# Kernel optimization log

Hardware: AMD Instinct MI355X
Metric: run time of the kernel (lower is better)

The kernel has to match this reference:

```python
import jax, jax.numpy as jnp
import numpy as np

B, N, C = 4, 4096, 1024
NUM_HEADS = 16
HEAD_DIM = C // NUM_HEADS


def setup_inputs() -> dict:
    key = jax.random.key(0)
    k1, k2, k3, k4 = jax.random.split(key, 4)
    s_in = 1.0 / np.sqrt(C)
    return {
        "x": jax.random.normal(k1, (B, N, C), dtype=jnp.float32),
        "H": 64,
        "W": 64,
        "Wqkv": jax.random.normal(k2, (3 * C, C), dtype=jnp.float32) * s_in,
        "Wproj": jax.random.normal(k3, (C, C), dtype=jnp.float32) * s_in,
        "bproj": jnp.zeros((C,), dtype=jnp.float32),
        "alpha": jnp.ones((NUM_HEADS,), dtype=jnp.float32),
    }


def reference(x, H, W, Wqkv, Wproj, bproj, alpha):
    Bb, Nn, Cc = x.shape
    h, d = NUM_HEADS, HEAD_DIM
    # qkv: [B, N, 3C] -> [3, B, h, N, d]
    qkv = jnp.einsum('bnc,oc->bno', x, Wqkv)
    qkv = qkv.reshape(Bb, Nn, 3, h, d).transpose(2, 0, 3, 1, 4)
    q, k, v = qkv[0], qkv[1], qkv[2]  # each [B, h, N, d]
    # channel attention: contract over tokens N -> [B, h, d, d]
    attn = jnp.einsum('bhnd,bhne->bhde', k, q) / alpha[None, :, None, None]
    attn = jax.nn.softmax(attn, axis=-1)
    # (dropout is identity in eval/reference mode)
    # head_out: [B, h, d, N] -> transpose -> [B, N, h, d] -> concat heads
    out = jnp.einsum('bhde,bhne->bhdn', attn, v)
    out = out.transpose(0, 3, 1, 2).reshape(Bb, Nn, Cc)
    return jnp.einsum('bnc,oc->bno', out, Wproj) + bproj
```

## Files before the change

kernel.cpp:

```cpp
#include <hip/hip_runtime.h>
#include <hip/hip_bf16.h>
#include <cstdint>
#include <cstddef>

typedef unsigned short u16;
typedef __bf16 bf16x8 __attribute__((ext_vector_type(8)));
typedef float f32x4 __attribute__((ext_vector_type(4)));
typedef unsigned short u16x4 __attribute__((ext_vector_type(4)));
typedef unsigned short u16x8 __attribute__((ext_vector_type(8)));

#define AS1(p) ((__attribute__((address_space(1))) void*)(p))
#define AS3(p) ((__attribute__((address_space(3))) void*)(p))

__device__ __forceinline__ float bf2f(u16 u) {
  unsigned v = ((unsigned)u) << 16; float f; __builtin_memcpy(&f, &v, 4); return f;
}
__device__ __forceinline__ u16 f2bf(float f) {
  unsigned u; __builtin_memcpy(&u, &f, 4);
  u += 0x7FFFu + ((u >> 16) & 1u);
  return (u16)(u >> 16);
}

__global__ __launch_bounds__(256) void convert_kernel(const float* __restrict__ src,
                                                      u16* __restrict__ dst, int n4) {
  int i = blockIdx.x * blockDim.x + threadIdx.x;
  int stride = gridDim.x * blockDim.x;
  for (; i < n4; i += stride) {
    float4 v = ((const float4*)src)[i];
    u16x4 o;
    o.x = f2bf(v.x); o.y = f2bf(v.y); o.z = f2bf(v.z); o.w = f2bf(v.w);
    ((u16x4*)dst)[i] = o;
  }
}

__global__ __launch_bounds__(256) void convert_split_kernel(const float* __restrict__ src,
                                                            u16* __restrict__ hi,
                                                            u16* __restrict__ lo, int n4) {
  int i = blockIdx.x * blockDim.x + threadIdx.x;
  int stride = gridDim.x * blockDim.x;
  for (; i < n4; i += stride) {
    float4 v = ((const float4*)src)[i];
    u16x4 oh, ol;
    oh.x = f2bf(v.x); ol.x = f2bf(v.x - bf2f(oh.x));
    oh.y = f2bf(v.y); ol.y = f2bf(v.y - bf2f(oh.y));
    oh.z = f2bf(v.z); ol.z = f2bf(v.z - bf2f(oh.z));
    oh.w = f2bf(v.w); ol.w = f2bf(v.w - bf2f(oh.w));
    ((u16x4*)hi)[i] = oh;
    ((u16x4*)lo)[i] = ol;
  }
}

__global__ __launch_bounds__(256) void transpose_split_kernel(const float* __restrict__ x,
                                                              u16* __restrict__ Xb,
                                                              u16* __restrict__ XThi,
                                                              u16* __restrict__ XTlo) {
  __shared__ u16 lhi[64 * 72];
  __shared__ u16 llo[64 * 72];
  const int t  = threadIdx.x;
  const int nT = blockIdx.x, cT = blockIdx.y, b = blockIdx.z;
  const size_t xbase = ((size_t)b * 4096 + nT * 64) * 1024 + cT * 64;
  const int c4 = (t & 15) * 4;
  const int r0 = t >> 4;
#pragma unroll
  for (int j = 0; j < 4; ++j) {
    int r = r0 + j * 16;
    float4 v = *(const float4*)(x + xbase + (size_t)r * 1024 + c4);
    u16x4 hi;
    hi.x = f2bf(v.x); hi.y = f2bf(v.y); hi.z = f2bf(v.z); hi.w = f2bf(v.w);
    *(u16x4*)(Xb + xbase + (size_t)r * 1024 + c4) = hi;
    u16 lo[4];
    lo[0] = f2bf(v.x - bf2f(hi.x)); lo[1] = f2bf(v.y - bf2f(hi.y));
    lo[2] = f2bf(v.z - bf2f(hi.z)); lo[3] = f2bf(v.w - bf2f(hi.w));
    u16 hia[4] = { hi.x, hi.y, hi.z, hi.w };
#pragma unroll
    for (int i = 0; i < 4; ++i) {
      lhi[(c4 + i) * 72 + r] = hia[i];
      llo[(c4 + i) * 72 + r] = lo[i];
    }
  }
  __syncthreads();
  const int c  = t >> 2;
  const int n0 = (t & 3) * 16;
  const size_t tbase = ((size_t)b * 1024 + cT * 64 + c) * 4096 + nT * 64 + n0;
  *(u16x8*)(XThi + tbase)     = *(const u16x8*)(lhi + c * 72 + n0);
  *(u16x8*)(XThi + tbase + 8) = *(const u16x8*)(lhi + c * 72 + n0 + 8);
  *(u16x8*)(XTlo + tbase)     = *(const u16x8*)(llo + c * 72 + n0);
  *(u16x8*)(XTlo + tbase + 8) = *(const u16x8*)(llo + c * 72 + n0 + 8);
}

template<bool OUT_BF16, bool HAS_BIAS>
__global__ __launch_bounds__(512, 2) void gemm_pipe(const u16* __restrict__ A,
                                                    const u16* __restrict__ B,
                                                    void* __restrict__ Cv,
                                                    const float* __restrict__ bias,
                                                    int M, int N, int K,
                                                    size_t sA, size_t sB, size_t sC) {
  __shared__ __align__(16) u16 lds[4][2][8192];
  const int tid  = threadIdx.x;
  const int lane = tid & 63;
  const int wave = tid >> 6;
  const int wm = wave >> 2, wn = wave & 3;
  const int rowTile = blockIdx.x * 256;
  const int colTile = blockIdx.y * 256;
  A += (size_t)blockIdx.z * sA;
  B += (size_t)blockIdx.z * sB;

  size_t srcA[2], srcB[2];
  int ldsOff[2];
#pragma unroll
  for (int j = 0; j < 2; ++j) {
    const int L = j * 512 + tid;
    const int sr = L >> 3;
    const int slot = (L & 7) ^ (sr & 7);
    const int r  = (sr << 1) | (slot >> 2);
    const int kq = slot & 3;
    srcA[j] = (size_t)(rowTile + r) * K + kq * 8;
    srcB[j] = (size_t)(colTile + r) * K + kq * 8;
    ldsOff[j] = (j * 512 + (tid & 448)) * 16;
  }

  const int m15 = lane & 15, kq4 = lane >> 4;
  const int r0a = wm * 128 + m15, sa0 = r0a >> 1;
  const int idxA0 = sa0 * 64 + (((((r0a & 1) << 2) | kq4)) ^ (sa0 & 7)) * 8;
  const int r0b = wn * 64 + m15, sb0 = r0b >> 1;
  const int idxB0 = sb0 * 64 + (((((r0b & 1) << 2) | kq4)) ^ (sb0 & 7)) * 8;

  const int NT = K >> 5;

  auto stageA = [&](int tt) {
    char* d = (char*)&lds[tt & 3][0][0];
    const int kt = tt << 5;
#pragma unroll
    for (int j = 0; j < 2; ++j)
      __builtin_amdgcn_global_load_lds(AS1(A + srcA[j] + kt), AS3(d + ldsOff[j]), 16, 0, 0);
  };
  auto stageB = [&](int tt) {
    char* d = (char*)&lds[tt & 3][1][0];
    const int kt = tt << 5;
#pragma unroll
    for (int j = 0; j < 2; ++j)
      __builtin_amdgcn_global_load_lds(AS1(B + srcB[j] + kt), AS3(d + ldsOff[j]), 16, 0, 0);
  };

  stageA(0); stageB(0);
  if (NT > 1) { stageA(1); stageB(1); }
  if (NT > 2) { stageA(2); stageB(2); }
  if (NT > 2) asm volatile("s_waitcnt vmcnt(8)" ::: "memory");
  else        asm volatile("s_waitcnt vmcnt(0)" ::: "memory");
  __builtin_amdgcn_sched_barrier(0);
  __builtin_amdgcn_s_barrier();
  __builtin_amdgcn_sched_barrier(0);

  f32x4 acc[8][4] = {};
  for (int t = 0; t < NT; ++t) {
    const u16* bufA = &lds[t & 3][0][0];
    const u16* bufB = &lds[t & 3][1][0];
    bf16x8 a[8], bfr[4];
#pragma unroll
    for (int ni = 0; ni < 4; ++ni) bfr[ni] = *(const bf16x8*)(bufB + idxB0 + ni * 512);
#pragma unroll
    for (int mi = 0; mi < 4; ++mi) a[mi] = *(const bf16x8*)(bufA + idxA0 + mi * 512);
    if (t + 3 < NT) stageA(t + 3);
    __builtin_amdgcn_sched_barrier(0);
    __builtin_amdgcn_s_barrier();
    __builtin_amdgcn_sched_barrier(0);
    __builtin_amdgcn_s_setprio(1);
#pragma unroll
    for (int mi = 0; mi < 4; ++mi)
#pragma unroll
      for (int ni = 0; ni < 4; ++ni)
        acc[mi][ni] = __builtin_amdgcn_mfma_f32_16x16x32_bf16(a[mi], bfr[ni], acc[mi][ni], 0, 0, 0);
    __builtin_amdgcn_s_setprio(0);
    __builtin_amdgcn_sched_barrier(0);
    __builtin_amdgcn_s_barrier();
    __builtin_amdgcn_sched_barrier(0);
#pragma unroll
    for (int mi = 4; mi < 8; ++mi) a[mi] = *(const bf16x8*)(bufA + idxA0 + mi * 512);
    if (t + 3 < NT) stageB(t + 3);
    __builtin_amdgcn_sched_barrier(0);
    __builtin_amdgcn_s_barrier();
    __builtin_amdgcn_sched_barrier(0);
    __builtin_amdgcn_s_setprio(1);
#pragma unroll
    for (int mi = 4; mi < 8; ++mi)
#pragma unroll
      for (int ni = 0; ni < 4; ++ni)
        acc[mi][ni] = __builtin_amdgcn_mfma_f32_16x16x32_bf16(a[mi], bfr[ni], acc[mi][ni], 0, 0, 0);
    __builtin_amdgcn_s_setprio(0);
    if (t < NT - 1) {
      if (t + 3 < NT)      asm volatile("s_waitcnt vmcnt(8)" ::: "memory");
      else if (t + 2 < NT) asm volatile("s_waitcnt vmcnt(4)" ::: "memory");
      else                 asm volatile("s_waitcnt vmcnt(0)" ::: "memory");
    }
    __builtin_amdgcn_sched_barrier(0);
    __builtin_amdgcn_s_barrier();
    __builtin_amdgcn_sched_barrier(0);
  }

  const int crow0 = rowTile + wm * 128 + (lane >> 4) * 4;
  const int ccol0 = colTile + wn * 64 + m15;
  if constexpr (OUT_BF16) {
    u16* C = (u16*)Cv + (size_t)blockIdx.z * sC;
#pragma unroll
    for (int mi = 0; mi < 8; ++mi)
#pragma unroll
      for (int ni = 0; ni < 4; ++ni) {
        const int col = ccol0 + ni * 16;
        const float bv = HAS_BIAS ? bias[col] : 0.f;
#pragma unroll
        for (int r = 0; r < 4; ++r)
          C[(size_t)(crow0 + mi * 16 + r) * N + col] = f2bf(acc[mi][ni][r] + bv);
      }
  } else {
    float* C = (float*)Cv + (size_t)blockIdx.z * sC;
#pragma unroll
    for (int mi = 0; mi < 8; ++mi)
#pragma unroll
      for (int ni = 0; ni < 4; ++ni) {
        const int col = ccol0 + ni * 16;
        const float bv = HAS_BIAS ? bias[col] : 0.f;
#pragma unroll
        for (int r = 0; r < 4; ++r)
          C[(size_t)(crow0 + mi * 16 + r) * N + col] = acc[mi][ni][r] + bv;
      }
  }
}

__global__ __launch_bounds__(256) void gemm_gram(const u16* __restrict__ XThi,
                                                 const u16* __restrict__ XTlo,
                                                 float* __restrict__ Gpart) {
  __shared__ __align__(16) u16 lAh[128 * 32];
  __shared__ __align__(16) u16 lAl[128 * 32];
  __shared__ __align__(16) u16 lBh[128 * 32];
  __shared__ __align__(16) u16 lBl[128 * 32];
  const int tid  = threadIdx.x;
  const int lane = tid & 63;
  const int wave = tid >> 6;
  const int wr = (wave >> 1) * 64;
  const int wc = (wave & 1) * 64;
  const int m  = lane & 15;
  const int ko = (lane >> 4) * 8;

  const int jx = blockIdx.x;
  const int b  = blockIdx.y;
  int rT, cT, slice, k0, kend;
  if (jx < 112) {
    const int tile = jx >> 2, kq = jx & 3;
    int t = tile, rt = 0;
    while (t >= 7 - rt) { t -= 7 - rt; ++rt; }
    const int ct = rt + 1 + t;
    rT = rt; cT = ct;
    if (kq >= 2) { rT = ct; cT = rt; }
    slice = kq & 1;
    k0 = kq * 1024; kend = k0 + 1024;
  } else {
    const int j2 = jx - 112;
    rT = cT = j2 >> 1;
    slice = j2 & 1;
    k0 = slice * 2048; kend = k0 + 2048;
  }
  const int rowTile = rT * 128, colTile = cT * 128;

  const u16* Ahp = XThi + ((size_t)b << 22);
  const u16* Alp = XTlo + ((size_t)b << 22);

  f32x4 acc[4][4] = {};
  for (int kt = k0; kt < kend; kt += 32) {
#pragma unroll
    for (int i = 0; i < 2; ++i) {
      int idx = i * 256 + tid;
      int row = idx >> 2;
      int kc  = (idx & 3) * 8;
      int ldsOff = (i * 256 + (tid & 192)) * 16;
      size_t aoff = (size_t)(rowTile + row) * 4096 + kt + kc;
      size_t boff = (size_t)(colTile + row) * 4096 + kt + kc;
      __builtin_amdgcn_global_load_lds(AS1(Ahp + aoff), AS3((char*)lAh + ldsOff), 16, 0, 0);
      __builtin_amdgcn_global_load_lds(AS1(Alp + aoff), AS3((char*)lAl + ldsOff), 16, 0, 0);
      __builtin_amdgcn_global_load_lds(AS1(Ahp + boff), AS3((char*)lBh + ldsOff), 16, 0, 0);
      __builtin_amdgcn_global_load_lds(AS1(Alp + boff), AS3((char*)lBl + ldsOff), 16, 0, 0);
    }
    __syncthreads();
    bf16x8 ah[4], al[4], bh[4], bl[4];
#pragma unroll
    for (int rb = 0; rb < 4; ++rb) {
      ah[rb] = *(const bf16x8*)(lAh + (wr + rb * 16 + m) * 32 + ko);
      al[rb] = *(const bf16x8*)(lAl + (wr + rb * 16 + m) * 32 + ko);
    }
#pragma unroll
    for (int cb = 0; cb < 4; ++cb) {
      bh[cb] = *(const bf16x8*)(lBh + (wc + cb * 16 + m) * 32 + ko);
      bl[cb] = *(const bf16x8*)(lBl + (wc + cb * 16 + m) * 32 + ko);
    }
#pragma unroll
    for (int rb = 0; rb < 4; ++rb)
#pragma unroll
      for (int cb = 0; cb < 4; ++cb) {
        acc[rb][cb] = __builtin_amdgcn_mfma_f32_16x16x32_bf16(ah[rb], bh[cb], acc[rb][cb], 0, 0, 0);
        acc[rb][cb] = __builtin_amdgcn_mfma_f32_16x16x32_bf16(ah[rb], bl[cb], acc[rb][cb], 0, 0, 0);
        acc[rb][cb] = __builtin_amdgcn_mfma_f32_16x16x32_bf16(al[rb], bh[cb], acc[rb][cb], 0, 0, 0);
      }
    __syncthreads();
  }

  float* out = Gpart + ((size_t)(slice * 4 + b) << 20);
  const int crow0 = rowTile + wr + (lane >> 4) * 4;
  const int ccol0 = colTile + wc + (lane & 15);
#pragma unroll
  for (int rb = 0; rb < 4; ++rb)
#pragma unroll
    for (int cb = 0; cb < 4; ++cb)
#pragma unroll
      for (int r = 0; r < 4; ++r)
        out[(size_t)(crow0 + rb * 16 + r) * 1024 + ccol0 + cb * 16] = acc[rb][cb][r];
}

__global__ __launch_bounds__(256) void gram_reduce_split(const float* __restrict__ Gp,
                                                         u16* __restrict__ Ghi,
                                                         u16* __restrict__ Glo) {
  const int rt = blockIdx.x, ct = blockIdx.y, b = blockIdx.z;
  const bool diag128 = (rt >> 1) == (ct >> 1);
  const float* s0 = Gp + ((size_t)b << 20);
  const float* s1 = Gp + ((size_t)(4 + b) << 20);
  __shared__ float lT[64 * 68];
  const int t = threadIdx.x;
  const int r = t >> 2;
  const int c16 = (t & 3) * 16;

  if (!diag128) {
    const size_t bb = (size_t)(ct * 64 + r) * 1024 + rt * 64 + c16;
#pragma unroll
    for (int q = 0; q < 4; ++q) {
      float4 v0 = *(const float4*)(s0 + bb + q * 4);
      float4 v1 = *(const float4*)(s1 + bb + q * 4);
      float4 s = { v0.x + v1.x, v0.y + v1.y, v0.z + v1.z, v0.w + v1.w };
      *(float4*)(lT + r * 68 + c16 + q * 4) = s;
    }
    __syncthreads();
  }

  const size_t ab = (size_t)(rt * 64 + r) * 1024 + ct * 64 + c16;
  const size_t ob = ((size_t)b << 20) + ab;
#pragma unroll
  for (int q = 0; q < 4; ++q) {
    float4 v0 = *(const float4*)(s0 + ab + q * 4);
    float4 v1 = *(const float4*)(s1 + ab + q * 4);
    float g[4] = { v0.x + v1.x, v0.y + v1.y, v0.z + v1.z, v0.w + v1.w };
    if (!diag128) {
#pragma unroll
      for (int i = 0; i < 4; ++i) g[i] += lT[(c16 + q * 4 + i) * 68 + r];
    }
    u16x4 oh, ol;
    oh.x = f2bf(g[0]); ol.x = f2bf(g[0] - bf2f(oh.x));
    oh.y = f2bf(g[1]); ol.y = f2bf(g[1] - bf2f(oh.y));
    oh.z = f2bf(g[2]); ol.z = f2bf(g[2] - bf2f(oh.z));
    oh.w = f2bf(g[3]); ol.w = f2bf(g[3] - bf2f(oh.w));
    *(u16x4*)(Ghi + ob + q * 4) = oh;
    *(u16x4*)(Glo + ob + q * 4) = ol;
  }
}

__global__ __launch_bounds__(256) void gemm_tprime(const u16* __restrict__ Wqh,
                                                   const u16* __restrict__ Wql,
                                                   const u16* __restrict__ Ghi,
                                                   const u16* __restrict__ Glo,
                                                   u16* __restrict__ Tph,
                                                   u16* __restrict__ Tpl) {
  __shared__ __align__(16) u16 lAh[128 * 32];
  __shared__ __align__(16) u16 lAl[128 * 32];
  __shared__ __align__(16) u16 lBh[128 * 32];
  __shared__ __align__(16) u16 lBl[128 * 32];
  const int tid  = threadIdx.x;
  const int lane = tid & 63;
  const int wave = tid >> 6;
  const int rowTile = blockIdx.x * 128;
  const int colTile = blockIdx.y * 128;
  const size_t zoff = (size_t)blockIdx.z << 20;
  const int wr = (wave >> 1) * 64;
  const int wc = (wave & 1) * 64;

  f32x4 acc[4][4] = {};
  const int m  = lane & 15;
  const int ko = (lane >> 4) * 8;

  for (int kt = 0; kt < 1024; kt += 32) {
#pragma unroll
    for (int i = 0; i < 2; ++i) {
      int idx = i * 256 + tid;
      int row = idx >> 2;
      int kc  = (idx & 3) * 8;
      int ldsOff = (i * 256 + (tid & 192)) * 16;
      size_t aoff = (size_t)(rowTile + row) * 1024 + kt + kc;
      size_t boff = zoff + (size_t)(colTile + row) * 1024 + kt + kc;
      __builtin_amdgcn_global_load_lds(AS1(Wqh + aoff), AS3((char*)lAh + ldsOff), 16, 0, 0);
      __builtin_amdgcn_global_load_lds(AS1(Wql + aoff), AS3((char*)lAl + ldsOff), 16, 0, 0);
      __builtin_amdgcn_global_load_lds(AS1(Ghi + boff), AS3((char*)lBh + ldsOff), 16, 0, 0);
      __builtin_amdgcn_global_load_lds(AS1(Glo + boff), AS3((char*)lBl + ldsOff), 16, 0, 0);
    }
    __syncthreads();
    bf16x8 ah[4], al[4], bh[4], bl[4];
#pragma unroll
    for (int rb = 0; rb < 4; ++rb) {
      ah[rb] = *(const bf16x8*)(lAh + (wr + rb * 16 + m) * 32 + ko);
      al[rb] = *(const bf16x8*)(lAl + (wr + rb * 16 + m) * 32 + ko);
    }
#pragma unroll
    for (int cb = 0; cb < 4; ++cb) {
      bh[cb] = *(const bf16x8*)(lBh + (wc + cb * 16 + m) * 32 + ko);
      bl[cb] = *(const bf16x8*)(lBl + (wc + cb * 16 + m) * 32 + ko);
    }
#pragma unroll
    for (int rb = 0; rb < 4; ++rb)
#pragma unroll
      for (int cb = 0; cb < 4; ++cb) {
        acc[rb][cb] = __builtin_amdgcn_mfma_f32_16x16x32_bf16(ah[rb], bh[cb], acc[rb][cb], 0, 0, 0);
        acc[rb][cb] = __builtin_amdgcn_mfma_f32_16x16x32_bf16(ah[rb], bl[cb], acc[rb][cb], 0, 0, 0);
        acc[rb][cb] = __builtin_amdgcn_mfma_f32_16x16x32_bf16(al[rb], bh[cb], acc[rb][cb], 0, 0, 0);
      }
    __syncthreads();
  }

  const int crow0 = rowTile + wr + (lane >> 4) * 4;
  const int ccol0 = colTile + wc + (lane & 15);
#pragma unroll
  for (int rb = 0; rb < 4; ++rb)
#pragma unroll
    for (int cb = 0; cb < 4; ++cb)
#pragma unroll
      for (int r = 0; r < 4; ++r) {
        float v = acc[rb][cb][r];
        u16 hi = f2bf(v);
        u16 lo = f2bf(v - bf2f(hi));
        size_t off = zoff + (size_t)(crow0 + rb * 16 + r) * 1024 + ccol0 + cb * 16;
        Tph[off] = hi;
        Tpl[off] = lo;
      }
}

__global__ __launch_bounds__(256) void s_softmax_kernel(const u16* __restrict__ Wqh,
                                                        const u16* __restrict__ Wql,
                                                        const u16* __restrict__ Tph,
                                                        const u16* __restrict__ Tpl,
                                                        const float* __restrict__ alpha,
                                                        u16* __restrict__ attnT) {
  const int h = blockIdx.x, b = blockIdx.y;
  const int tid = threadIdx.x, lane = tid & 63, wave = tid >> 6;
  __shared__ __align__(16) u16 lAh[64 * 32];
  __shared__ __align__(16) u16 lAl[64 * 32];
  __shared__ __align__(16) u16 lBh[64 * 32];
  __shared__ __align__(16) u16 lBl[64 * 32];

  const size_t aBase = (size_t)(1024 + h * 64) * 1024;
  const size_t bBase = ((size_t)b << 20) + (size_t)(h * 64) * 1024;

  f32x4 acc[4] = {};
  const int m  = lane & 15;
  const int ko = (lane >> 4) * 8;
  const int srow = tid >> 2;
  const int skc  = (tid & 3) * 8;
  const int ldsOff = (tid & 192) * 16;

  for (int kt = 0; kt < 1024; kt += 32) {
    __builtin_amdgcn_global_load_lds(AS1(Wqh + aBase + (size_t)srow * 1024 + kt + skc),
                                     AS3((char*)lAh + ldsOff), 16, 0, 0);
    __builtin_amdgcn_global_load_lds(AS1(Wql + aBase + (size_t)srow * 1024 + kt + skc),
                                     AS3((char*)lAl + ldsOff), 16, 0, 0);
    __builtin_amdgcn_global_load_lds(AS1(Tph + bBase + (size_t)srow * 1024 + kt + skc),
                                     AS3((char*)lBh + ldsOff), 16, 0, 0);
    __builtin_amdgcn_global_load_lds(AS1(Tpl + bBase + (size_t)srow * 1024 + kt + skc),
                                     AS3((char*)lBl + ldsOff), 16, 0, 0);
    __syncthreads();
    bf16x8 ah = *(const bf16x8*)(lAh + (wave * 16 + m) * 32 + ko);
    bf16x8 al = *(const bf16x8*)(lAl + (wave * 16 + m) * 32 + ko);
#pragma unroll
    for (int cb = 0; cb < 4; ++cb) {
      bf16x8 bh = *(const bf16x8*)(lBh + (cb * 16 + m) * 32 + ko);
      bf16x8 bl = *(const bf16x8*)(lBl + (cb * 16 + m) * 32 + ko);
      acc[cb] = __builtin_amdgcn_mfma_f32_16x16x32_bf16(ah, bh, acc[cb], 0, 0, 0);
      acc[cb] = __builtin_amdgcn_mfma_f32_16x16x32_bf16(ah, bl, acc[cb], 0, 0, 0);
      acc[cb] = __builtin_amdgcn_mfma_f32_16x16x32_bf16(al, bh, acc[cb], 0, 0, 0);
    }
    __syncthreads();
  }

  const float invA = 1.f / alpha[h];
  const int g = lane >> 4;
  const size_t obase = (size_t)(b * 16 + h) * 4096;
#pragma unroll
  for (int r = 0; r < 4; ++r) {
    int d = wave * 16 + g * 4 + r;
    float s[4];
#pragma unroll
    for (int cb = 0; cb < 4; ++cb) s[cb] = acc[cb][r] * invA;
    float mx = fmaxf(fmaxf(s[0], s[1]), fmaxf(s[2], s[3]));
#pragma unroll
    for (int o = 1; o < 16; o <<= 1) mx = fmaxf(mx, __shfl_xor(mx, o, 64));
    float e[4]; float sum = 0.f;
#pragma unroll
    for (int cb = 0; cb < 4; ++cb) { e[cb] = __expf(s[cb] - mx); sum += e[cb]; }
#pragma unroll
    for (int o = 1; o < 16; o <<= 1) sum += __shfl_xor(sum, o, 64);
    float inv = 1.f / sum;
#pragma unroll
    for (int cb = 0; cb < 4; ++cb) {
      int e_idx = cb * 16 + (lane & 15);
      attnT[obase + (size_t)e_idx * 64 + d] = f2bf(e[cb] * inv);
    }
  }
}

__global__ __launch_bounds__(256) void m_build_kernel(const u16* __restrict__ Wpb,
                                                      const u16* __restrict__ attnT,
                                                      u16* __restrict__ Mb) {
  const int oT = blockIdx.x, h = blockIdx.y, b = blockIdx.z;
  const int tid = threadIdx.x, lane = tid & 63, wave = tid >> 6;
  __shared__ __align__(16) u16 lA[128 * 64];
  __shared__ __align__(16) u16 lB[64 * 64];
  const int bh = b * 16 + h;
#pragma unroll
  for (int i = 0; i < 4; ++i) {
    int idx = i * 256 + tid;
    int row = idx >> 3;
    int kc  = (idx & 7) * 8;
    int ldsOff = (i * 256 + (tid & 192)) * 16;
    __builtin_amdgcn_global_load_lds(AS1(Wpb + (size_t)(oT * 128 + row) * 1024 + h * 64 + kc),
                                     AS3((char*)lA + ldsOff), 16, 0, 0);
  }
#pragma unroll
  for (int i = 0; i < 2; ++i) {
    int idx = i * 256 + tid;
    int ldsOff = (i * 256 + (tid & 192)) * 16;
    __builtin_amdgcn_global_load_lds(AS1(attnT + (size_t)bh * 4096 + idx * 8),
                                     AS3((char*)lB + ldsOff), 16, 0, 0);
  }
  __syncthreads();
  const int m  = lane & 15;
  const int ko = (lane >> 4) * 8;
  const int wr = wave * 32;
  f32x4 acc[2][4] = {};
#pragma unroll
  for (int ks = 0; ks < 2; ++ks) {
#pragma unroll
    for (int rb = 0; rb < 2; ++rb) {
      bf16x8 a = *(const bf16x8*)(lA + (wr + rb * 16 + m) * 64 + ks * 32 + ko);
#pragma unroll
      for (int cb = 0; cb < 4; ++cb) {
        bf16x8 bb = *(const bf16x8*)(lB + (cb * 16 + m) * 64 + ks * 32 + ko);
        acc[rb][cb] = __builtin_amdgcn_mfma_f32_16x16x32_bf16(a, bb, acc[rb][cb], 0, 0, 0);
      }
    }
  }
  u16* out = Mb + ((size_t)b << 20);
#pragma unroll
  for (int rb = 0; rb < 2; ++rb)
#pragma unroll
    for (int cb = 0; cb < 4; ++cb) {
      int col = h * 64 + cb * 16 + (lane & 15);
#pragma unroll
      for (int r = 0; r < 4; ++r) {
        int row = oT * 128 + wr + rb * 16 + (lane >> 4) * 4 + r;
        out[(size_t)row * 1024 + col] = f2bf(acc[rb][cb][r]);
      }
    }
}

extern "C" void kernel_launch(void* const* d_in, const int* in_sizes, int n_in,
                              void* d_out, int out_size, void* d_ws, size_t ws_size,
                              hipStream_t stream) {
  const float* x     = (const float*)d_in[0];
  const float* Wqkv  = (const float*)d_in[3];
  const float* Wproj = (const float*)d_in[4];
  const float* bproj = (const float*)d_in[5];
  const float* alpha = (const float*)d_in[6];

  char* ws = (char*)d_ws;
  u16*   Xb     = (u16*)ws;
  float* Gpart  = (float*)ws;
  u16*   Mb     = (u16*)ws;
  u16*   XThi   = (u16*)(ws + 33554432);
  u16*   attnTb = (u16*)(ws + 33554432);
  u16*   XTlo  = (u16*)(ws + 67108864);
  u16*   Ghi   = (u16*)(ws + 67108864);
  u16*   Glo   = (u16*)(ws + 75497472);
  u16*   Tph   = (u16*)(ws + 83886080);
  u16*   Tpl   = (u16*)(ws + 92274688);
  u16*   Wqh   = (u16*)(ws + 100663296);
  u16*   Wql   = (u16*)(ws + 106954752);
  u16*   Vb    = (u16*)(ws + 113246208);
  u16*   Wpb   = (u16*)(ws + 146800640);

  transpose_split_kernel<<<dim3(64, 16, 4), 256, 0, stream>>>(x, Xb, XThi, XTlo);
  convert_split_kernel<<<256, 256, 0, stream>>>(Wqkv, Wqh, Wql, 3145728 / 4);
  convert_kernel<<<128, 256, 0, stream>>>(Wproj, Wpb, 1048576 / 4);
  gemm_pipe<true, false><<<dim3(64, 4, 1), 512, 0, stream>>>(
      Xb, Wqh + (size_t)2048 * 1024, Vb, nullptr, 16384, 1024, 1024,
      (size_t)0, (size_t)0, (size_t)0);
  gemm_gram<<<dim3(128, 4), 256, 0, stream>>>(XThi, XTlo, Gpart);
  gram_reduce_split<<<dim3(16, 16, 4), 256, 0, stream>>>(Gpart, Ghi, Glo);
  gemm_tprime<<<dim3(8, 8, 4), 256, 0, stream>>>(Wqh, Wql, Ghi, Glo, Tph, Tpl);
  s_softmax_kernel<<<dim3(16, 4), 256, 0, stream>>>(Wqh, Wql, Tph, Tpl, alpha, attnTb);
  m_build_kernel<<<dim3(8, 16, 4), 256, 0, stream>>>(Wpb, attnTb, Mb);
  gemm_pipe<false, true><<<dim3(16, 4, 4), 512, 0, stream>>>(
      Vb, Mb, (float*)d_out, bproj, 4096, 1024, 1024,
      (size_t)1 << 22, (size_t)1 << 20, (size_t)1 << 22);
}
```

Before: 422.4 us.

## Replace gram and T' GEMMs with 4-stage pipelined, swizzled 512-thread kernels

New measurement: 381.8 us. 1.11x faster.

```diff
diff --git a/kernel.cpp b/kernel.cpp
--- a/kernel.cpp
+++ b/kernel.cpp
@@ -226,92 +226,145 @@
   }
 }
 
-__global__ __launch_bounds__(256) void gemm_gram(const u16* __restrict__ XThi,
-                                                 const u16* __restrict__ XTlo,
-                                                 float* __restrict__ Gpart) {
-  __shared__ __align__(16) u16 lAh[128 * 32];
-  __shared__ __align__(16) u16 lAl[128 * 32];
-  __shared__ __align__(16) u16 lBh[128 * 32];
-  __shared__ __align__(16) u16 lBl[128 * 32];
-  const int tid  = threadIdx.x;
-  const int lane = tid & 63;
-  const int wave = tid >> 6;
-  const int wr = (wave >> 1) * 64;
-  const int wc = (wave & 1) * 64;
-  const int m  = lane & 15;
-  const int ko = (lane >> 4) * 8;
-
-  const int jx = blockIdx.x;
-  const int b  = blockIdx.y;
-  int rT, cT, slice, k0, kend;
-  if (jx < 112) {
-    const int tile = jx >> 2, kq = jx & 3;
+__device__ __forceinline__ void pipe4_core(const u16* __restrict__ pAh,
+                                           const u16* __restrict__ pAl,
+                                           const u16* __restrict__ pBh,
+                                           const u16* __restrict__ pBl,
+                                           u16* lds, int ldsByteOff,
+                                           int idxA0, int idxB0, int NT,
+                                           f32x4 acc[4][2]) {
+  auto stage2A = [&](int tt) {
+    u16* d = lds + (tt & 3) * 16384;
+    const int kt = tt << 5;
+    __builtin_amdgcn_global_load_lds(AS1(pAh + kt), AS3((char*)d + ldsByteOff), 16, 0, 0);
+    __builtin_amdgcn_global_load_lds(AS1(pAl + kt), AS3((char*)(d + 4096) + ldsByteOff), 16, 0, 0);
+  };
+  auto stage2B = [&](int tt) {
+    u16* d = lds + (tt & 3) * 16384 + 8192;
+    const int kt = tt << 5;
+    __builtin_amdgcn_global_load_lds(AS1(pBh + kt), AS3((char*)d + ldsByteOff), 16, 0, 0);
+    __builtin_amdgcn_global_load_lds(AS1(pBl + kt), AS3((char*)(d + 4096) + ldsByteOff), 16, 0, 0);
+  };
+
+  stage2A(0); stage2B(0);
+  stage2A(1); stage2B(1);
+  stage2A(2); stage2B(2);
+  asm volatile("s_waitcnt vmcnt(8)" ::: "memory");
+  __builtin_amdgcn_sched_barrier(0);
+  __builtin_amdgcn_s_barrier();
+  __builtin_amdgcn_sched_barrier(0);
+
+  for (int t = 0; t < NT; ++t) {
+    const u16* base = lds + (t & 3) * 16384;
+    bf16x8 ah[4], al[4], bh[2], bl[2];
+    bh[0] = *(const bf16x8*)(base + 8192 + idxB0);
+    bh[1] = *(const bf16x8*)(base + 8192 + idxB0 + 512);
+    bl[0] = *(const bf16x8*)(base + 12288 + idxB0);
+    bl[1] = *(const bf16x8*)(base + 12288 + idxB0 + 512);
+    ah[0] = *(const bf16x8*)(base + idxA0);
+    ah[1] = *(const bf16x8*)(base + idxA0 + 512);
+    al[0] = *(const bf16x8*)(base + 4096 + idxA0);
+    al[1] = *(const bf16x8*)(base + 4096 + idxA0 + 512);
+    if (t + 3 < NT) stage2A(t + 3);
+    __builtin_amdgcn_sched_barrier(0);
+    __builtin_amdgcn_s_barrier();
+    __builtin_amdgcn_sched_barrier(0);
+    __builtin_amdgcn_s_setprio(1);
+#pragma unroll
+    for (int mi = 0; mi < 2; ++mi)
+#pragma unroll
+      for (int ni = 0; ni < 2; ++ni) {
+        acc[mi][ni] = __builtin_amdgcn_mfma_f32_16x16x32_bf16(ah[mi], bh[ni], acc[mi][ni], 0, 0, 0);
+        acc[mi][ni] = __builtin_amdgcn_mfma_f32_16x16x32_bf16(ah[mi], bl[ni], acc[mi][ni], 0, 0, 0);
+        acc[mi][ni] = __builtin_amdgcn_mfma_f32_16x16x32_bf16(al[mi], bh[ni], acc[mi][ni], 0, 0, 0);
+      }
+    __builtin_amdgcn_s_setprio(0);
+    __builtin_amdgcn_sched_barrier(0);
+    __builtin_amdgcn_s_barrier();
+    __builtin_amdgcn_sched_barrier(0);
+    ah[2] = *(const bf16x8*)(base + idxA0 + 1024);
+    ah[3] = *(const bf16x8*)(base + idxA0 + 1536);
+    al[2] = *(const bf16x8*)(base + 4096 + idxA0 + 1024);
+    al[3] = *(const bf16x8*)(base + 4096 + idxA0 + 1536);
+    if (t + 3 < NT) stage2B(t + 3);
+    __builtin_amdgcn_sched_barrier(0);
+    __builtin_amdgcn_s_barrier();
+    __builtin_amdgcn_sched_barrier(0);
+    __builtin_amdgcn_s_setprio(1);
+#pragma unroll
+    for (int mi = 2; mi < 4; ++mi)
+#pragma unroll
+      for (int ni = 0; ni < 2; ++ni) {
+        acc[mi][ni] = __builtin_amdgcn_mfma_f32_16x16x32_bf16(ah[mi], bh[ni], acc[mi][ni], 0, 0, 0);
+        acc[mi][ni] = __builtin_amdgcn_mfma_f32_16x16x32_bf16(ah[mi], bl[ni], acc[mi][ni], 0, 0, 0);
+        acc[mi][ni] = __builtin_amdgcn_mfma_f32_16x16x32_bf16(al[mi], bh[ni], acc[mi][ni], 0, 0, 0);
+      }
+    __builtin_amdgcn_s_setprio(0);
+    if (t < NT - 1) {
+      if (t + 3 < NT)      asm volatile("s_waitcnt vmcnt(8)" ::: "memory");
+      else if (t + 2 < NT) asm volatile("s_waitcnt vmcnt(4)" ::: "memory");
+      else                 asm volatile("s_waitcnt vmcnt(0)" ::: "memory");
+    }
+    __builtin_amdgcn_sched_barrier(0);
+    __builtin_amdgcn_s_barrier();
+    __builtin_amdgcn_sched_barrier(0);
+  }
+}
+
+__global__ __launch_bounds__(512, 2) void gram_pipe(const u16* __restrict__ XThi,
+                                                    const u16* __restrict__ XTlo,
+                                                    float* __restrict__ Gpart) {
+  __shared__ __align__(16) u16 lds[4 * 4 * 4096];
+  const int tid = threadIdx.x, lane = tid & 63, wave = tid >> 6;
+  const int wm = wave >> 2, wn = wave & 3;
+  const int bid = blockIdx.x;
+  int b, rT, cT, slice, k0, NT;
+  if (bid < 64) {
+    b = bid & 3; const int j = bid >> 2;
+    rT = cT = j >> 1; slice = j & 1; k0 = slice * 2048; NT = 64;
+  } else {
+    const int e = bid - 64; b = e & 3;
+    const int idx = e >> 2; const int tile = idx >> 2, kq = idx & 3;
     int t = tile, rt = 0;
     while (t >= 7 - rt) { t -= 7 - rt; ++rt; }
     const int ct = rt + 1 + t;
     rT = rt; cT = ct;
     if (kq >= 2) { rT = ct; cT = rt; }
-    slice = kq & 1;
-    k0 = kq * 1024; kend = k0 + 1024;
-  } else {
-    const int j2 = jx - 112;
-    rT = cT = j2 >> 1;
-    slice = j2 & 1;
-    k0 = slice * 2048; kend = k0 + 2048;
+    slice = kq & 1; k0 = kq * 1024; NT = 32;
   }
   const int rowTile = rT * 128, colTile = cT * 128;
-
-  const u16* Ahp = XThi + ((size_t)b << 22);
-  const u16* Alp = XTlo + ((size_t)b << 22);
-
-  f32x4 acc[4][4] = {};
-  for (int kt = k0; kt < kend; kt += 32) {
-#pragma unroll
-    for (int i = 0; i < 2; ++i) {
-      int idx = i * 256 + tid;
-      int row = idx >> 2;
-      int kc  = (idx & 3) * 8;
-      int ldsOff = (i * 256 + (tid & 192)) * 16;
-      size_t aoff = (size_t)(rowTile + row) * 4096 + kt + kc;
-      size_t boff = (size_t)(colTile + row) * 4096 + kt + kc;
-      __builtin_amdgcn_global_load_lds(AS1(Ahp + aoff), AS3((char*)lAh + ldsOff), 16, 0, 0);
-      __builtin_amdgcn_global_load_lds(AS1(Alp + aoff), AS3((char*)lAl + ldsOff), 16, 0, 0);
-      __builtin_amdgcn_global_load_lds(AS1(Ahp + boff), AS3((char*)lBh + ldsOff), 16, 0, 0);
-      __builtin_amdgcn_global_load_lds(AS1(Alp + boff), AS3((char*)lBl + ldsOff), 16, 0, 0);
-    }
-    __syncthreads();
-    bf16x8 ah[4], al[4], bh[4], bl[4];
-#pragma unroll
-    for (int rb = 0; rb < 4; ++rb) {
-      ah[rb] = *(const bf16x8*)(lAh + (wr + rb * 16 + m) * 32 + ko);
-      al[rb] = *(const bf16x8*)(lAl + (wr + rb * 16 + m) * 32 + ko);
-    }
-#pragma unroll
-    for (int cb = 0; cb < 4; ++cb) {
-      bh[cb] = *(const bf16x8*)(lBh + (wc + cb * 16 + m) * 32 + ko);
-      bl[cb] = *(const bf16x8*)(lBl + (wc + cb * 16 + m) * 32 + ko);
-    }
-#pragma unroll
-    for (int rb = 0; rb < 4; ++rb)
-#pragma unroll
-      for (int cb = 0; cb < 4; ++cb) {
-        acc[rb][cb] = __builtin_amdgcn_mfma_f32_16x16x32_bf16(ah[rb], bh[cb], acc[rb][cb], 0, 0, 0);
-        acc[rb][cb] = __builtin_amdgcn_mfma_f32_16x16x32_bf16(ah[rb], bl[cb], acc[rb][cb], 0, 0, 0);
-        acc[rb][cb] = __builtin_amdgcn_mfma_f32_16x16x32_bf16(al[rb], bh[cb], acc[rb][cb], 0, 0, 0);
-      }
-    __syncthreads();
-  }
+  const u16* Ah = XThi + ((size_t)b << 22);
+  const u16* Al = XTlo + ((size_t)b << 22);
+
+  const int sr = tid >> 3;
+  const int slot = (tid & 7) ^ (sr & 7);
+  const int r = (sr << 1) | (slot >> 2);
+  const int kq8 = (slot & 3) * 8;
+  const u16* pAh = Ah + (size_t)(rowTile + r) * 4096 + k0 + kq8;
+  const u16* pAl = Al + (size_t)(rowTile + r) * 4096 + k0 + kq8;
+  const u16* pBh = Ah + (size_t)(colTile + r) * 4096 + k0 + kq8;
+  const u16* pBl = Al + (size_t)(colTile + r) * 4096 + k0 + kq8;
+  const int ldsByteOff = (tid & 448) * 16;
+
+  const int m15 = lane & 15, kq4 = lane >> 4;
+  const int r0a = wm * 64 + m15, sa0 = r0a >> 1;
+  const int idxA0 = sa0 * 64 + (((((r0a & 1) << 2) | kq4)) ^ (sa0 & 7)) * 8;
+  const int r0b = wn * 32 + m15, sb0 = r0b >> 1;
+  const int idxB0 = sb0 * 64 + (((((r0b & 1) << 2) | kq4)) ^ (sb0 & 7)) * 8;
+
+  f32x4 acc[4][2] = {};
+  pipe4_core(pAh, pAl, pBh, pBl, lds, ldsByteOff, idxA0, idxB0, NT, acc);
 
   float* out = Gpart + ((size_t)(slice * 4 + b) << 20);
-  const int crow0 = rowTile + wr + (lane >> 4) * 4;
-  const int ccol0 = colTile + wc + (lane & 15);
-#pragma unroll
-  for (int rb = 0; rb < 4; ++rb)
-#pragma unroll
-    for (int cb = 0; cb < 4; ++cb)
-#pragma unroll
-      for (int r = 0; r < 4; ++r)
-        out[(size_t)(crow0 + rb * 16 + r) * 1024 + ccol0 + cb * 16] = acc[rb][cb][r];
+  const int crow0 = rowTile + wm * 64 + (lane >> 4) * 4;
+  const int ccol0 = colTile + wn * 32 + m15;
+#pragma unroll
+  for (int mi = 0; mi < 4; ++mi)
+#pragma unroll
+    for (int ni = 0; ni < 2; ++ni)
+#pragma unroll
+      for (int r4 = 0; r4 < 4; ++r4)
+        out[(size_t)(crow0 + mi * 16 + r4) * 1024 + ccol0 + ni * 16] = acc[mi][ni][r4];
 }
 
 __global__ __launch_bounds__(256) void gram_reduce_split(const float* __restrict__ Gp,
@@ -359,78 +412,51 @@
   }
 }
 
-__global__ __launch_bounds__(256) void gemm_tprime(const u16* __restrict__ Wqh,
-                                                   const u16* __restrict__ Wql,
-                                                   const u16* __restrict__ Ghi,
-                                                   const u16* __restrict__ Glo,
-                                                   u16* __restrict__ Tph,
-                                                   u16* __restrict__ Tpl) {
-  __shared__ __align__(16) u16 lAh[128 * 32];
-  __shared__ __align__(16) u16 lAl[128 * 32];
-  __shared__ __align__(16) u16 lBh[128 * 32];
-  __shared__ __align__(16) u16 lBl[128 * 32];
-  const int tid  = threadIdx.x;
-  const int lane = tid & 63;
-  const int wave = tid >> 6;
-  const int rowTile = blockIdx.x * 128;
-  const int colTile = blockIdx.y * 128;
-  const size_t zoff = (size_t)blockIdx.z << 20;
-  const int wr = (wave >> 1) * 64;
-  const int wc = (wave & 1) * 64;
-
-  f32x4 acc[4][4] = {};
-  const int m  = lane & 15;
-  const int ko = (lane >> 4) * 8;
-
-  for (int kt = 0; kt < 1024; kt += 32) {
-#pragma unroll
-    for (int i = 0; i < 2; ++i) {
-      int idx = i * 256 + tid;
-      int row = idx >> 2;
-      int kc  = (idx & 3) * 8;
-      int ldsOff = (i * 256 + (tid & 192)) * 16;
-      size_t aoff = (size_t)(rowTile + row) * 1024 + kt + kc;
-      size_t boff = zoff + (size_t)(colTile + row) * 1024 + kt + kc;
-      __builtin_amdgcn_global_load_lds(AS1(Wqh + aoff), AS3((char*)lAh + ldsOff), 16, 0, 0);
-      __builtin_amdgcn_global_load_lds(AS1(Wql + aoff), AS3((char*)lAl + ldsOff), 16, 0, 0);
-      __builtin_amdgcn_global_load_lds(AS1(Ghi + boff), AS3((char*)lBh + ldsOff), 16, 0, 0);
-      __builtin_amdgcn_global_load_lds(AS1(Glo + boff), AS3((char*)lBl + ldsOff), 16, 0, 0);
-    }
-    __syncthreads();
-    bf16x8 ah[4], al[4], bh[4], bl[4];
-#pragma unroll
-    for (int rb = 0; rb < 4; ++rb) {
-      ah[rb] = *(const bf16x8*)(lAh + (wr + rb * 16 + m) * 32 + ko);
-      al[rb] = *(const bf16x8*)(lAl + (wr + rb * 16 + m) * 32 + ko);
-    }
-#pragma unroll
-    for (int cb = 0; cb < 4; ++cb) {
-      bh[cb] = *(const bf16x8*)(lBh + (wc + cb * 16 + m) * 32 + ko);
-      bl[cb] = *(const bf16x8*)(lBl + (wc + cb * 16 + m) * 32 + ko);
-    }
-#pragma unroll
-    for (int rb = 0; rb < 4; ++rb)
-#pragma unroll
-      for (int cb = 0; cb < 4; ++cb) {
-        acc[rb][cb] = __builtin_amdgcn_mfma_f32_16x16x32_bf16(ah[rb], bh[cb], acc[rb][cb], 0, 0, 0);
-        acc[rb][cb] = __builtin_amdgcn_mfma_f32_16x16x32_bf16(ah[rb], bl[cb], acc[rb][cb], 0, 0, 0);
-        acc[rb][cb] = __builtin_amdgcn_mfma_f32_16x16x32_bf16(al[rb], bh[cb], acc[rb][cb], 0, 0, 0);
-      }
-    __syncthreads();
-  }
-
-  const int crow0 = rowTile + wr + (lane >> 4) * 4;
-  const int ccol0 = colTile + wc + (lane & 15);
-#pragma unroll
-  for (int rb = 0; rb < 4; ++rb)
-#pragma unroll
-    for (int cb = 0; cb < 4; ++cb)
-#pragma unroll
-      for (int r = 0; r < 4; ++r) {
-        float v = acc[rb][cb][r];
+__global__ __launch_bounds__(512, 2) void tprime_pipe(const u16* __restrict__ Wqh,
+                                                      const u16* __restrict__ Wql,
+                                                      const u16* __restrict__ Ghi,
+                                                      const u16* __restrict__ Glo,
+                                                      u16* __restrict__ Tph,
+                                                      u16* __restrict__ Tpl) {
+  __shared__ __align__(16) u16 lds[4 * 4 * 4096];
+  const int tid = threadIdx.x, lane = tid & 63, wave = tid >> 6;
+  const int wm = wave >> 2, wn = wave & 3;
+  const int bid = blockIdx.x;
+  const int b = bid & 3, tile = bid >> 2;
+  const int rowTile = (tile >> 3) * 128, colTile = (tile & 7) * 128;
+  const size_t zoff = (size_t)b << 20;
+
+  const int sr = tid >> 3;
+  const int slot = (tid & 7) ^ (sr & 7);
+  const int r = (sr << 1) | (slot >> 2);
+  const int kq8 = (slot & 3) * 8;
+  const u16* pAh = Wqh + (size_t)(rowTile + r) * 1024 + kq8;
+  const u16* pAl = Wql + (size_t)(rowTile + r) * 1024 + kq8;
+  const u16* pBh = Ghi + zoff + (size_t)(colTile + r) * 1024 + kq8;
+  const u16* pBl = Glo + zoff + (size_t)(colTile + r) * 1024 + kq8;
+  const int ldsByteOff = (tid & 448) * 16;
+
+  const int m15 = lane & 15, kq4 = lane >> 4;
+  const int r0a = wm * 64 + m15, sa0 = r0a >> 1;
+  const int idxA0 = sa0 * 64 + (((((r0a & 1) << 2) | kq4)) ^ (sa0 & 7)) * 8;
+  const int r0b = wn * 32 + m15, sb0 = r0b >> 1;
+  const int idxB0 = sb0 * 64 + (((((r0b & 1) << 2) | kq4)) ^ (sb0 & 7)) * 8;
+
+  f32x4 acc[4][2] = {};
+  pipe4_core(pAh, pAl, pBh, pBl, lds, ldsByteOff, idxA0, idxB0, 32, acc);
+
+  const int crow0 = rowTile + wm * 64 + (lane >> 4) * 4;
+  const int ccol0 = colTile + wn * 32 + m15;
+#pragma unroll
+  for (int mi = 0; mi < 4; ++mi)
+#pragma unroll
+    for (int ni = 0; ni < 2; ++ni)
+#pragma unroll
+      for (int r4 = 0; r4 < 4; ++r4) {
+        float v = acc[mi][ni][r4];
         u16 hi = f2bf(v);
         u16 lo = f2bf(v - bf2f(hi));
-        size_t off = zoff + (size_t)(crow0 + rb * 16 + r) * 1024 + ccol0 + cb * 16;
+        size_t off = zoff + (size_t)(crow0 + mi * 16 + r4) * 1024 + ccol0 + ni * 16;
         Tph[off] = hi;
         Tpl[off] = lo;
       }
@@ -594,9 +620,9 @@
   gemm_pipe<true, false><<<dim3(64, 4, 1), 512, 0, stream>>>(
       Xb, Wqh + (size_t)2048 * 1024, Vb, nullptr, 16384, 1024, 1024,
       (size_t)0, (size_t)0, (size_t)0);
-  gemm_gram<<<dim3(128, 4), 256, 0, stream>>>(XThi, XTlo, Gpart);
+  gram_pipe<<<dim3(512), 512, 0, stream>>>(XThi, XTlo, Gpart);
   gram_reduce_split<<<dim3(16, 16, 4), 256, 0, stream>>>(Gpart, Ghi, Glo);
-  gemm_tprime<<<dim3(8, 8, 4), 256, 0, stream>>>(Wqh, Wql, Ghi, Glo, Tph, Tpl);
+  tprime_pipe<<<dim3(256), 512, 0, stream>>>(Wqh, Wql, Ghi, Glo, Tph, Tpl);
   s_softmax_kernel<<<dim3(16, 4), 256, 0, stream>>>(Wqh, Wql, Tph, Tpl, alpha, attnTb);
   m_build_kernel<<<dim3(8, 16, 4), 256, 0, stream>>>(Wpb, attnTb, Mb);
   gemm_pipe<false, true><<<dim3(16, 4, 4), 512, 0, stream>>>(
```
